# Kernel tuning notes

Measured on AMD Instinct MI355X. Metric: run time of the kernel, lower is better.

Reference implementation:

```python
import jax, jax.numpy as jnp
import numpy as np

B, L, D = 2, 2048, 2048
NH, HD = 16, 128
SCALE = HD ** -0.5


def setup_inputs() -> dict:
    key = jax.random.key(0)
    ks = jax.random.split(key, 9)
    s = D ** -0.5  # roughly torch Linear init scale
    return {
        "hidden_states": jax.random.normal(ks[0], (B, L, D), dtype=jnp.float32),
        "Wq": jax.random.normal(ks[1], (NH * HD, D), dtype=jnp.float32) * s,
        "bq": jnp.zeros((NH * HD,), dtype=jnp.float32),
        "Wk": jax.random.normal(ks[2], (NH * HD, D), dtype=jnp.float32) * s,
        "bk": jnp.zeros((NH * HD,), dtype=jnp.float32),
        "Wv": jax.random.normal(ks[3], (NH * HD, D), dtype=jnp.float32) * s,
        "bv": jnp.zeros((NH * HD,), dtype=jnp.float32),
        "Wo": jax.random.normal(ks[4], (D, NH * HD), dtype=jnp.float32) * s,
        "bo": jnp.zeros((D,), dtype=jnp.float32),
    }


def reference(hidden_states, Wq, bq, Wk, bk, Wv, bv, Wo, bo):
    # projections (torch Linear: x @ W.T + b), split into heads: b s h d
    q = (hidden_states @ Wq.T + bq).reshape(B, L, NH, HD)
    k = (hidden_states @ Wk.T + bk).reshape(B, L, NH, HD)
    v = (hidden_states @ Wv.T + bv).reshape(B, L, NH, HD)
    # scores: [B, NH, L, L]
    scores = jnp.einsum("bqhd,bkhd->bhqk", q, k) * SCALE
    causal = jnp.tril(jnp.ones((L, L), dtype=bool))  # True = keep
    scores = jnp.where(causal, scores, jnp.float32(-jnp.inf))
    probs = jax.nn.softmax(scores, axis=-1)
    out = jnp.einsum("bhqk,bkhd->bqhd", probs, v).reshape(B, L, NH * HD)
    return out @ Wo.T + bo
```

## Files before the change

### kernel.cpp

```cpp
#include <hip/hip_runtime.h>

#define B_  2
#define L_  2048
#define D_  2048
#define NH_ 16
#define HD_ 128

typedef __bf16 bf16_t;
typedef __bf16 bf16x8 __attribute__((ext_vector_type(8)));
typedef __bf16 bf16x4 __attribute__((ext_vector_type(4)));
typedef float  f32x4  __attribute__((ext_vector_type(4)));

typedef const __attribute__((address_space(1))) void* gas_ptr;
typedef __attribute__((address_space(3))) void* las_ptr;

__device__ __forceinline__ void g2l16(const void* g, void* l) {
    __builtin_amdgcn_global_load_lds((gas_ptr)g, (las_ptr)l, 16, 0, 0);
}

__device__ __forceinline__ void raw_barrier() {
    asm volatile("s_barrier" ::: "memory");
}
__device__ __forceinline__ void wait_vm8() {
    asm volatile("s_waitcnt vmcnt(8)" ::: "memory");
}
__device__ __forceinline__ void wait_vm4() {
    asm volatile("s_waitcnt vmcnt(4)" ::: "memory");
}
__device__ __forceinline__ void wait_vm2() {
    asm volatile("s_waitcnt vmcnt(2)" ::: "memory");
}
__device__ __forceinline__ void wait_vm0() {
    asm volatile("s_waitcnt vmcnt(0)" ::: "memory");
}

__global__ __launch_bounds__(256) void cvt_all(const float* __restrict__ X,
                                               const float* __restrict__ Wq,
                                               const float* __restrict__ Wk,
                                               const float* __restrict__ Wv,
                                               const float* __restrict__ Wo,
                                               bf16_t* __restrict__ Xb,
                                               bf16_t* __restrict__ Wqkvb,
                                               bf16_t* __restrict__ Wob) {
    int i = blockIdx.x * 256 + threadIdx.x;
    const float* src;
    bf16_t* dst;
    int off;
    if (i < 2097152) { src = X; dst = Xb; off = i; }
    else {
        int j = i - 2097152;
        int w = j >> 20;
        off = j & 1048575;
        src = (w == 0) ? Wq : (w == 1) ? Wk : (w == 2) ? Wv : Wo;
        dst = (w == 3) ? Wob : Wqkvb + (size_t)w * 4194304;
    }
    float4 v = ((const float4*)src)[off];
    bf16x4 o;
    o[0] = (bf16_t)v.x; o[1] = (bf16_t)v.y; o[2] = (bf16_t)v.z; o[3] = (bf16_t)v.w;
    ((bf16x4*)dst)[off] = o;
}

__global__ __launch_bounds__(256) void gemm_bt(const bf16_t* __restrict__ A,
                                               const bf16_t* __restrict__ Bw,
                                               const float* __restrict__ bias,
                                               float* __restrict__ C,
                                               int M, int N, int K) {
    constexpr int BK = 32;
    __shared__ __align__(16) bf16_t smem[16384];
    const int tid  = threadIdx.x;
    const int wave = tid >> 6, lane = tid & 63;
    const int quad = lane >> 4, l16 = lane & 15;
    const int tm = blockIdx.y * 128, tn = blockIdx.x * 128;
    const int wm = (wave >> 1) * 64, wn = (wave & 1) * 64;

    const int srow = wave * 16 + (lane >> 2);
    const int scol = (lane & 3) * 8;
    const bf16_t* Ag = A  + (size_t)(tm + srow) * K + scol;
    const bf16_t* Bg = Bw + (size_t)(tn + srow) * K + scol;
    const size_t rowskip = (size_t)64 * K;

    auto stage = [&](int k0, int p) {
        bf16_t* a = smem + p * 4096 + (wave * 16) * BK;
        bf16_t* bl = smem + 8192 + p * 4096 + (wave * 16) * BK;
        g2l16(Ag + k0, a);
        g2l16(Ag + k0 + rowskip, a + 64 * BK);
        g2l16(Bg + k0, bl);
        g2l16(Bg + k0 + rowskip, bl + 64 * BK);
    };

    f32x4 acc[4][4] = {};
    const int niter = K / BK;
    stage(0, 0);

    for (int i = 0; i < niter; ++i) {
        const int p = i & 1;
        if (i + 1 < niter) { stage((i + 1) * BK, p ^ 1); wait_vm4(); }
        else wait_vm0();
        raw_barrier();

        const bf16_t* Alp = smem + p * 4096;
        const bf16_t* Blp = smem + 8192 + p * 4096;
        bf16x8 af[4], bf[4];
#pragma unroll
        for (int ii = 0; ii < 4; ++ii)
            af[ii] = *(const bf16x8*)(Alp + (wm + ii * 16 + l16) * BK + quad * 8);
#pragma unroll
        for (int j = 0; j < 4; ++j)
            bf[j] = *(const bf16x8*)(Blp + (wn + j * 16 + l16) * BK + quad * 8);
#pragma unroll
        for (int ii = 0; ii < 4; ++ii)
#pragma unroll
            for (int j = 0; j < 4; ++j)
                acc[ii][j] = __builtin_amdgcn_mfma_f32_16x16x32_bf16(af[ii], bf[j], acc[ii][j], 0, 0, 0);
        raw_barrier();
    }

#pragma unroll
    for (int j = 0; j < 4; ++j) {
        const int col = tn + wn + j * 16 + l16;
        const float bv = bias[col];
#pragma unroll
        for (int i = 0; i < 4; ++i) {
            const int row0 = tm + wm + i * 16 + quad * 4;
#pragma unroll
            for (int r = 0; r < 4; ++r)
                C[(size_t)(row0 + r) * N + col] = acc[i][j][r] + bv;
        }
    }
}

__global__ __launch_bounds__(512, 2) void gemm_qk(const bf16_t* __restrict__ A,
                                                  const bf16_t* __restrict__ Bw,
                                                  const float* __restrict__ b0,
                                                  const float* __restrict__ b1,
                                                  bf16_t* __restrict__ QK) {
    constexpr int K  = D_;
    constexpr int BK = 64;
    constexpr int NT = K / BK;
    __shared__ __align__(16) bf16_t smem[65536];

    const int tid  = threadIdx.x;
    const int wave = tid >> 6, lane = tid & 63;
    const int quad = lane >> 4, l16 = lane & 15;
    const int tm = blockIdx.y * 256, tn = blockIdx.x * 256;
    const int wm = (wave >> 2) * 128;
    const int wn = (wave & 3) * 64;
    const int seg = tn >> 11;

    const int srow = tid >> 3;
    const int sg   = (tid & 7) ^ (srow & 7);
    const bf16_t* Ag = A  + (size_t)(tm + srow) * K + sg * 8;
    const bf16_t* Bg = Bw + (size_t)(tn + srow) * K + sg * 8;
    const int ldsw = wave * 512;

    auto stageA = [&](int t, int h) {
        bf16_t* l = smem + (t & 1) * 32768 + h * 8192 + ldsw;
        const bf16_t* g = Ag + (size_t)h * 128 * K + t * BK;
        g2l16(g, l);
        g2l16(g + (size_t)64 * K, l + 4096);
    };
    auto stageB = [&](int t, int h) {
        bf16_t* l = smem + (t & 1) * 32768 + 16384 + h * 8192 + ldsw;
        const bf16_t* g = Bg + (size_t)h * 128 * K + t * BK;
        g2l16(g, l);
        g2l16(g + (size_t)64 * K, l + 4096);
    };

    f32x4 acc[8][4] = {};

    stageA(0, 0); stageA(0, 1); stageB(0, 0); stageB(0, 1);

    const int abase_w = (wave >> 2) * 8192;
    const int bbase_w = 16384 + ((wave >> 1) & 1) * 8192;
    const int brow0   = (wave & 1) * 64;

    for (int t = 0; t < NT; ++t) {
        const int p = t & 1;
        const bf16_t* Ah = smem + p * 32768 + abase_w;
        const bf16_t* Bh = smem + p * 32768 + bbase_w;
        bf16x8 af[4][2], bfr[2][2], bfr2[2][2];

        raw_barrier();
        if (t + 1 < NT) { stageA(t + 1, 0); wait_vm2(); }
        else wait_vm0();
        raw_barrier();

#pragma unroll
        for (int mb = 0; mb < 4; ++mb)
#pragma unroll
            for (int ks = 0; ks < 2; ++ks) {
                const int row = mb * 16 + l16;
                af[mb][ks] = *(const bf16x8*)(Ah + row * 64 + (((ks * 4 + quad) ^ (row & 7)) << 3));
            }
#pragma unroll
        for (int nb = 0; nb < 2; ++nb)
#pragma unroll
            for (int ks = 0; ks < 2; ++ks) {
                const int row = brow0 + nb * 16 + l16;
                bfr[nb][ks] = *(const bf16x8*)(Bh + row * 64 + (((ks * 4 + quad) ^ (row & 7)) << 3));
            }
        __builtin_amdgcn_s_setprio(1);
#pragma unroll
        for (int mb = 0; mb < 4; ++mb)
#pragma unroll
            for (int nb = 0; nb < 2; ++nb)
#pragma unroll
                for (int ks = 0; ks < 2; ++ks)
                    acc[mb][nb] = __builtin_amdgcn_mfma_f32_16x16x32_bf16(af[mb][ks], bfr[nb][ks], acc[mb][nb], 0, 0, 0);
        __builtin_amdgcn_s_setprio(0);

        if (t + 1 < NT) stageA(t + 1, 1);
#pragma unroll
        for (int nb = 0; nb < 2; ++nb)
#pragma unroll
            for (int ks = 0; ks < 2; ++ks) {
                const int row = brow0 + (nb + 2) * 16 + l16;
                bfr2[nb][ks] = *(const bf16x8*)(Bh + row * 64 + (((ks * 4 + quad) ^ (row & 7)) << 3));
            }
        raw_barrier();
        __builtin_amdgcn_s_setprio(1);
#pragma unroll
        for (int mb = 0; mb < 4; ++mb)
#pragma unroll
            for (int nb = 0; nb < 2; ++nb)
#pragma unroll
                for (int ks = 0; ks < 2; ++ks)
                    acc[mb][nb + 2] = __builtin_amdgcn_mfma_f32_16x16x32_bf16(af[mb][ks], bfr2[nb][ks], acc[mb][nb + 2], 0, 0, 0);
        __builtin_amdgcn_s_setprio(0);

        if (t + 1 < NT) stageB(t + 1, 0);
#pragma unroll
        for (int mb = 0; mb < 4; ++mb)
#pragma unroll
            for (int ks = 0; ks < 2; ++ks) {
                const int row = (mb + 4) * 16 + l16;
                af[mb][ks] = *(const bf16x8*)(Ah + row * 64 + (((ks * 4 + quad) ^ (row & 7)) << 3));
            }
        raw_barrier();
        __builtin_amdgcn_s_setprio(1);
#pragma unroll
        for (int mb = 0; mb < 4; ++mb)
#pragma unroll
            for (int nb = 0; nb < 2; ++nb)
#pragma unroll
                for (int ks = 0; ks < 2; ++ks)
                    acc[mb + 4][nb + 2] = __builtin_amdgcn_mfma_f32_16x16x32_bf16(af[mb][ks], bfr2[nb][ks], acc[mb + 4][nb + 2], 0, 0, 0);
        __builtin_amdgcn_s_setprio(0);

        if (t + 1 < NT) stageB(t + 1, 1);
#pragma unroll
        for (int nb = 0; nb < 2; ++nb)
#pragma unroll
            for (int ks = 0; ks < 2; ++ks) {
                const int row = brow0 + nb * 16 + l16;
                bfr[nb][ks] = *(const bf16x8*)(Bh + row * 64 + (((ks * 4 + quad) ^ (row & 7)) << 3));
            }
        raw_barrier();
        __builtin_amdgcn_s_setprio(1);
#pragma unroll
        for (int mb = 0; mb < 4; ++mb)
#pragma unroll
            for (int nb = 0; nb < 2; ++nb)
#pragma unroll
                for (int ks = 0; ks < 2; ++ks)
                    acc[mb + 4][nb] = __builtin_amdgcn_mfma_f32_16x16x32_bf16(af[mb][ks], bfr[nb][ks], acc[mb + 4][nb], 0, 0, 0);
        __builtin_amdgcn_s_setprio(0);
    }

    const float* bias = (seg == 0) ? b0 : b1;
#pragma unroll
    for (int nb = 0; nb < 4; ++nb) {
        const int col = tn + wn + nb * 16 + l16;
        const float bv = bias[col & 2047];
#pragma unroll
        for (int mb = 0; mb < 8; ++mb) {
            const int row0 = tm + wm + mb * 16 + quad * 4;
#pragma unroll
            for (int r = 0; r < 4; ++r)
                QK[(size_t)(row0 + r) * 4096 + col] = (bf16_t)(acc[mb][nb][r] + bv);
        }
    }
}

__global__ __launch_bounds__(512, 2) void gemm_v(const bf16_t* __restrict__ A,
                                                 const bf16_t* __restrict__ Bv,
                                                 const float* __restrict__ b2,
                                                 bf16_t* __restrict__ Vt) {
    constexpr int K  = D_;
    constexpr int BK = 64;
    constexpr int NT = K / BK;
    __shared__ __align__(16) bf16_t smem[49152];

    const int tid  = threadIdx.x;
    const int wave = tid >> 6, lane = tid & 63;
    const int quad = lane >> 4, l16 = lane & 15;
    const int hx = blockIdx.x;
    const int tm = blockIdx.y * 256;
    const int wm = (wave >> 1) * 64;
    const int wn = (wave & 1) * 64;

    const int srow = tid >> 3;
    const int sg   = (tid & 7) ^ (srow & 7);
    const bf16_t* Ag = A  + (size_t)(tm + srow) * K + sg * 8;
    const bf16_t* Bg = Bv + (size_t)(hx * 128 + srow) * K + sg * 8;
    const int ldsw = wave * 512;

    auto stageVA = [&](int t, int q) {
        bf16_t* l = smem + (t & 1) * 24576 + q * 4096 + ldsw;
        g2l16(Ag + (size_t)q * 64 * K + t * BK, l);
    };
    auto stageVB = [&](int t, int q) {
        bf16_t* l = smem + (t & 1) * 24576 + 16384 + q * 4096 + ldsw;
        g2l16(Bg + (size_t)q * 64 * K + t * BK, l);
    };

    f32x4 acc[4][4] = {};

    stageVA(0, 0); stageVA(0, 1); stageVA(0, 2); stageVA(0, 3);
    stageVB(0, 0); stageVB(0, 1);

    for (int t = 0; t < NT; ++t) {
        const int p = t & 1;
        const bf16_t* Ah = smem + p * 24576;
        const bf16_t* Bl = smem + p * 24576 + 16384;
        bf16x8 af0[4], af1[4], bf0[2], bf1[2], bf2[2], bf3[2];

        raw_barrier();
        if (t + 1 < NT) { stageVA(t + 1, 0); stageVA(t + 1, 1); wait_vm2(); }
        else wait_vm0();
        raw_barrier();

#pragma unroll
        for (int mb = 0; mb < 4; ++mb) {
            const int row = wm + mb * 16 + l16;
            af0[mb] = *(const bf16x8*)(Ah + row * 64 + ((quad ^ (row & 7)) << 3));
        }
#pragma unroll
        for (int nb = 0; nb < 2; ++nb) {
            const int row = wn + nb * 16 + l16;
            bf0[nb] = *(const bf16x8*)(Bl + row * 64 + ((quad ^ (row & 7)) << 3));
        }
        __builtin_amdgcn_s_setprio(1);
#pragma unroll
        for (int mb = 0; mb < 4; ++mb)
#pragma unroll
            for (int nb = 0; nb < 2; ++nb)
                acc[mb][nb] = __builtin_amdgcn_mfma_f32_16x16x32_bf16(af0[mb], bf0[nb], acc[mb][nb], 0, 0, 0);
        __builtin_amdgcn_s_setprio(0);

        if (t + 1 < NT) { stageVA(t + 1, 2); stageVB(t + 1, 0); }
#pragma unroll
        for (int nb = 0; nb < 2; ++nb) {
            const int row = wn + (nb + 2) * 16 + l16;
            bf1[nb] = *(const bf16x8*)(Bl + row * 64 + ((quad ^ (row & 7)) << 3));
        }
        raw_barrier();
        __builtin_amdgcn_s_setprio(1);
#pragma unroll
        for (int mb = 0; mb < 4; ++mb)
#pragma unroll
            for (int nb = 0; nb < 2; ++nb)
                acc[mb][nb + 2] = __builtin_amdgcn_mfma_f32_16x16x32_bf16(af0[mb], bf1[nb], acc[mb][nb + 2], 0, 0, 0);
        __builtin_amdgcn_s_setprio(0);

        if (t + 1 < NT) { stageVA(t + 1, 3); stageVB(t + 1, 1); }
#pragma unroll
        for (int mb = 0; mb < 4; ++mb) {
            const int row = wm + mb * 16 + l16;
            af1[mb] = *(const bf16x8*)(Ah + row * 64 + (((4 + quad) ^ (row & 7)) << 3));
        }
#pragma unroll
        for (int nb = 0; nb < 2; ++nb) {
            const int row = wn + (nb + 2) * 16 + l16;
            bf2[nb] = *(const bf16x8*)(Bl + row * 64 + (((4 + quad) ^ (row & 7)) << 3));
        }
        raw_barrier();
        __builtin_amdgcn_s_setprio(1);
#pragma unroll
        for (int mb = 0; mb < 4; ++mb)
#pragma unroll
            for (int nb = 0; nb < 2; ++nb)
                acc[mb][nb + 2] = __builtin_amdgcn_mfma_f32_16x16x32_bf16(af1[mb], bf2[nb], acc[mb][nb + 2], 0, 0, 0);
        __builtin_amdgcn_s_setprio(0);

#pragma unroll
        for (int nb = 0; nb < 2; ++nb) {
            const int row = wn + nb * 16 + l16;
            bf3[nb] = *(const bf16x8*)(Bl + row * 64 + (((4 + quad) ^ (row & 7)) << 3));
        }
        raw_barrier();
        __builtin_amdgcn_s_setprio(1);
#pragma unroll
        for (int mb = 0; mb < 4; ++mb)
#pragma unroll
            for (int nb = 0; nb < 2; ++nb)
                acc[mb][nb] = __builtin_amdgcn_mfma_f32_16x16x32_bf16(af1[mb], bf3[nb], acc[mb][nb], 0, 0, 0);
        __builtin_amdgcn_s_setprio(0);
    }

    __syncthreads();
    bf16_t* Tw = smem + wave * 4096;
    const int b = tm >> 11;
    const int tokbase = tm & 2047;
#pragma unroll
    for (int nb = 0; nb < 4; ++nb) {
        const int dloc = nb * 16 + l16;
        const float bv = b2[hx * 128 + wn + dloc];
#pragma unroll
        for (int mb = 0; mb < 4; ++mb)
#pragma unroll
            for (int r = 0; r < 4; ++r) {
                const int tokl = mb * 16 + quad * 4 + r;
                Tw[dloc * 64 + ((((tokl >> 3) ^ (dloc & 7)) << 3) | (tokl & 7))] =
                    (bf16_t)(acc[mb][nb][r] + bv);
            }
    }
    const int dl = lane;
    bf16_t* gp = Vt + ((size_t)(b * NH_ + hx) * HD_ + wn + dl) * L_ + tokbase + wm;
#pragma unroll
    for (int c = 0; c < 8; ++c) {
        bf16x8 v = *(const bf16x8*)(Tw + dl * 64 + ((c ^ (dl & 7)) << 3));
        *(bf16x8*)(gp + c * 8) = v;
    }
}

__global__ __launch_bounds__(256, 2) void attn_kernel(const bf16_t* __restrict__ QK,
                                                      const bf16_t* __restrict__ Vt,
                                                      bf16_t* __restrict__ Ctx) {
    constexpr float SCALE = 0.08838834764831845f;
    constexpr float MFIX  = 8.0f;
    const int bid = blockIdx.x;
    const int bh = bid & 31;
    const int qt = 15 - (bid >> 5);
    const int b = bh >> 4, h = bh & 15;
    const int tid = threadIdx.x, wave = tid >> 6, lane = tid & 63;
    const int quad = lane >> 4, l16 = lane & 15;
    const int q0 = qt * 128;

    __shared__ bf16_t Kl[2][64 * 128];
    __shared__ bf16_t Vl[2][128 * 64];
    __shared__ bf16_t Pl[4][16 * 72];

    bf16x8 qf[2][4];
#pragma unroll
    for (int s = 0; s < 2; ++s) {
        const bf16_t* qp = QK + (size_t)(b * L_ + q0 + wave * 32 + s * 16 + l16) * 4096 + h * HD_ + quad * 8;
#pragma unroll
        for (int ks = 0; ks < 4; ++ks) qf[s][ks] = *(const bf16x8*)(qp + ks * 32);
    }

    bf16x8 ones;
#pragma unroll
    for (int j = 0; j < 8; ++j) ones[j] = (bf16_t)1.0f;

    f32x4 oacc[2][8] = {};
    f32x4 lacc[2] = {};

    const bf16_t* Kg = QK + (size_t)(b * L_) * 4096 + 2048 + h * HD_;
    const bf16_t* Vg = Vt + (size_t)(bh * HD_) * L_;

    auto stage = [&](int tile, int p) {
        const bf16_t* kg = Kg + (size_t)tile * 64 * 4096;
        const bf16_t* vg = Vg + tile * 64;
#pragma unroll
        for (int c = 0; c < 4; ++c) {
            int row = c * 16 + wave * 4 + (lane >> 4);
            int gcol = ((lane & 15) ^ (row & 15)) * 8;
            g2l16(kg + (size_t)row * 4096 + gcol, &Kl[p][(c * 16 + wave * 4) * 128]);
        }
#pragma unroll
        for (int c = 0; c < 4; ++c) {
            int row = c * 32 + wave * 8 + (lane >> 3);
            int gcol = ((lane & 7) ^ (row & 7)) * 8;
            g2l16(vg + (size_t)row * L_ + gcol, &Vl[p][(c * 32 + wave * 8) * 64]);
        }
    };

    const int n = 2 * qt + 2;
    stage(0, 0);

    for (int it = 0; it < n; ++it) {
        const int p = it & 1;
        if (it + 1 < n) {
            stage(it + 1, p ^ 1);
            wait_vm8();
        } else {
            wait_vm0();
        }
        raw_barrier();

        const int kb = it * 64;
        const bool need_mask = (it >= n - 2);

        f32x4 sa[2][4] = {};
#pragma unroll
        for (int nt = 0; nt < 4; ++nt) {
            const int krow = nt * 16 + l16;
#pragma unroll
            for (int ks = 0; ks < 4; ++ks) {
                bf16x8 kf = *(const bf16x8*)(&Kl[p][krow * 128 + (((ks * 4 + quad) ^ l16) * 8)]);
                sa[0][nt] = __builtin_amdgcn_mfma_f32_16x16x32_bf16(qf[0][ks], kf, sa[0][nt], 0, 0, 0);
                sa[1][nt] = __builtin_amdgcn_mfma_f32_16x16x32_bf16(qf[1][ks], kf, sa[1][nt], 0, 0, 0);
            }
        }

        bf16x8 pf0[2], pf1[2];
#pragma unroll
        for (int nt = 0; nt < 4; ++nt)
#pragma unroll
            for (int r = 0; r < 4; ++r) {
                float sv = sa[0][nt][r] * SCALE - MFIX;
                if (need_mask) {
                    const int key = kb + nt * 16 + l16;
                    const int qq = q0 + wave * 32 + quad * 4 + r;
                    sv = (key <= qq) ? sv : -1e30f;
                }
                Pl[wave][(quad * 4 + r) * 72 + nt * 16 + l16] = (bf16_t)__expf(sv);
            }
        pf0[0] = *(const bf16x8*)(&Pl[wave][l16 * 72 + quad * 8]);
        pf0[1] = *(const bf16x8*)(&Pl[wave][l16 * 72 + 32 + quad * 8]);

#pragma unroll
        for (int nt = 0; nt < 4; ++nt)
#pragma unroll
            for (int r = 0; r < 4; ++r) {
                float sv = sa[1][nt][r] * SCALE - MFIX;
                if (need_mask) {
                    const int key = kb + nt * 16 + l16;
                    const int qq = q0 + wave * 32 + 16 + quad * 4 + r;
                    sv = (key <= qq) ? sv : -1e30f;
                }
                Pl[wave][(quad * 4 + r) * 72 + nt * 16 + l16] = (bf16_t)__expf(sv);
            }
        pf1[0] = *(const bf16x8*)(&Pl[wave][l16 * 72 + quad * 8]);
        pf1[1] = *(const bf16x8*)(&Pl[wave][l16 * 72 + 32 + quad * 8]);

        lacc[0] = __builtin_amdgcn_mfma_f32_16x16x32_bf16(pf0[0], ones, lacc[0], 0, 0, 0);
        lacc[0] = __builtin_amdgcn_mfma_f32_16x16x32_bf16(pf0[1], ones, lacc[0], 0, 0, 0);
        lacc[1] = __builtin_amdgcn_mfma_f32_16x16x32_bf16(pf1[0], ones, lacc[1], 0, 0, 0);
        lacc[1] = __builtin_amdgcn_mfma_f32_16x16x32_bf16(pf1[1], ones, lacc[1], 0, 0, 0);

#pragma unroll
        for (int dt = 0; dt < 8; ++dt) {
            const int drow = dt * 16 + l16;
#pragma unroll
            for (int ks = 0; ks < 2; ++ks) {
                bf16x8 vf = *(const bf16x8*)(&Vl[p][drow * 64 + (((ks * 4 + quad) ^ (drow & 7)) * 8)]);
                oacc[0][dt] = __builtin_amdgcn_mfma_f32_16x16x32_bf16(pf0[ks], vf, oacc[0][dt], 0, 0, 0);
                oacc[1][dt] = __builtin_amdgcn_mfma_f32_16x16x32_bf16(pf1[ks], vf, oacc[1][dt], 0, 0, 0);
            }
        }
        raw_barrier();
    }

#pragma unroll
    for (int s = 0; s < 2; ++s)
#pragma unroll
        for (int r = 0; r < 4; ++r) {
            const float inv = 1.0f / lacc[s][r];
            const int q = q0 + wave * 32 + s * 16 + quad * 4 + r;
            bf16_t* cp = Ctx + (size_t)(b * L_ + q) * 2048 + h * HD_;
#pragma unroll
            for (int dt = 0; dt < 8; ++dt)
                cp[dt * 16 + l16] = (bf16_t)(oacc[s][dt][r] * inv);
        }
}

extern "C" void kernel_launch(void* const* d_in, const int* in_sizes, int n_in,
                              void* d_out, int out_size, void* d_ws, size_t ws_size,
                              hipStream_t stream) {
    const float* X  = (const float*)d_in[0];
    const float* Wq = (const float*)d_in[1];
    const float* bq = (const float*)d_in[2];
    const float* Wk = (const float*)d_in[3];
    const float* bk = (const float*)d_in[4];
    const float* Wv = (const float*)d_in[5];
    const float* bv = (const float*)d_in[6];
    const float* Wo = (const float*)d_in[7];
    const float* bo = (const float*)d_in[8];
    float* out = (float*)d_out;

    char* ws = (char*)d_ws;
    bf16_t* Xb   = (bf16_t*)(ws);
    bf16_t* Ctx  = (bf16_t*)(ws);
    bf16_t* Wqkv = (bf16_t*)(ws + 16777216);
    bf16_t* Wob  = (bf16_t*)(ws + 41943040);
    bf16_t* QKb  = (bf16_t*)(ws + 50331648);
    bf16_t* Vtb  = (bf16_t*)(ws + 83886080);

    cvt_all<<<24576, 256, 0, stream>>>(X, Wq, Wk, Wv, Wo, Xb, Wqkv, Wob);

    gemm_qk<<<dim3(16, 16), 512, 0, stream>>>(Xb, Wqkv, bq, bk, QKb);

    gemm_v<<<dim3(16, 16), 512, 0, stream>>>(Xb, Wqkv + 8388608, bv, Vtb);

    attn_kernel<<<dim3(512), 256, 0, stream>>>(QKb, Vtb, Ctx);

    gemm_bt<<<dim3(16, 32), 256, 0, stream>>>(Ctx, Wob, bo, out,
                                              B_ * L_, D_, D_);
}
```

Baseline: 359.8 us.

## Replace output GEMM with pipelined swizzled kernel and streamline attention softmax

```diff
diff --git a/kernel.cpp b/kernel.cpp
--- a/kernel.cpp
+++ b/kernel.cpp
@@ -24,14 +24,17 @@
 __device__ __forceinline__ void wait_vm8() {
     asm volatile("s_waitcnt vmcnt(8)" ::: "memory");
 }
-__device__ __forceinline__ void wait_vm4() {
-    asm volatile("s_waitcnt vmcnt(4)" ::: "memory");
-}
 __device__ __forceinline__ void wait_vm2() {
     asm volatile("s_waitcnt vmcnt(2)" ::: "memory");
 }
 __device__ __forceinline__ void wait_vm0() {
     asm volatile("s_waitcnt vmcnt(0)" ::: "memory");
+}
+
+__device__ __forceinline__ float hw_exp2(float x) {
+    float r;
+    asm("v_exp_f32 %0, %1" : "=v"(r) : "v"(x));
+    return r;
 }
 
 __global__ __launch_bounds__(256) void cvt_all(const float* __restrict__ X,
@@ -60,75 +63,6 @@
     ((bf16x4*)dst)[off] = o;
 }
 
-__global__ __launch_bounds__(256) void gemm_bt(const bf16_t* __restrict__ A,
-                                               const bf16_t* __restrict__ Bw,
-                                               const float* __restrict__ bias,
-                                               float* __restrict__ C,
-                                               int M, int N, int K) {
-    constexpr int BK = 32;
-    __shared__ __align__(16) bf16_t smem[16384];
-    const int tid  = threadIdx.x;
-    const int wave = tid >> 6, lane = tid & 63;
-    const int quad = lane >> 4, l16 = lane & 15;
-    const int tm = blockIdx.y * 128, tn = blockIdx.x * 128;
-    const int wm = (wave >> 1) * 64, wn = (wave & 1) * 64;
-
-    const int srow = wave * 16 + (lane >> 2);
-    const int scol = (lane & 3) * 8;
-    const bf16_t* Ag = A  + (size_t)(tm + srow) * K + scol;
-    const bf16_t* Bg = Bw + (size_t)(tn + srow) * K + scol;
-    const size_t rowskip = (size_t)64 * K;
-
-    auto stage = [&](int k0, int p) {
-        bf16_t* a = smem + p * 4096 + (wave * 16) * BK;
-        bf16_t* bl = smem + 8192 + p * 4096 + (wave * 16) * BK;
-        g2l16(Ag + k0, a);
-        g2l16(Ag + k0 + rowskip, a + 64 * BK);
-        g2l16(Bg + k0, bl);
-        g2l16(Bg + k0 + rowskip, bl + 64 * BK);
-    };
-
-    f32x4 acc[4][4] = {};
-    const int niter = K / BK;
-    stage(0, 0);
-
-    for (int i = 0; i < niter; ++i) {
-        const int p = i & 1;
-        if (i + 1 < niter) { stage((i + 1) * BK, p ^ 1); wait_vm4(); }
-        else wait_vm0();
-        raw_barrier();
-
-        const bf16_t* Alp = smem + p * 4096;
-        const bf16_t* Blp = smem + 8192 + p * 4096;
-        bf16x8 af[4], bf[4];
-#pragma unroll
-        for (int ii = 0; ii < 4; ++ii)
-            af[ii] = *(const bf16x8*)(Alp + (wm + ii * 16 + l16) * BK + quad * 8);
-#pragma unroll
-        for (int j = 0; j < 4; ++j)
-            bf[j] = *(const bf16x8*)(Blp + (wn + j * 16 + l16) * BK + quad * 8);
-#pragma unroll
-        for (int ii = 0; ii < 4; ++ii)
-#pragma unroll
-            for (int j = 0; j < 4; ++j)
-                acc[ii][j] = __builtin_amdgcn_mfma_f32_16x16x32_bf16(af[ii], bf[j], acc[ii][j], 0, 0, 0);
-        raw_barrier();
-    }
-
-#pragma unroll
-    for (int j = 0; j < 4; ++j) {
-        const int col = tn + wn + j * 16 + l16;
-        const float bv = bias[col];
-#pragma unroll
-        for (int i = 0; i < 4; ++i) {
-            const int row0 = tm + wm + i * 16 + quad * 4;
-#pragma unroll
-            for (int r = 0; r < 4; ++r)
-                C[(size_t)(row0 + r) * N + col] = acc[i][j][r] + bv;
-        }
-    }
-}
-
 __global__ __launch_bounds__(512, 2) void gemm_qk(const bf16_t* __restrict__ A,
                                                   const bf16_t* __restrict__ Bw,
                                                   const float* __restrict__ b0,
@@ -143,8 +77,6 @@
     const int wave = tid >> 6, lane = tid & 63;
     const int quad = lane >> 4, l16 = lane & 15;
     const int tm = blockIdx.y * 256, tn = blockIdx.x * 256;
-    const int wm = (wave >> 2) * 128;
-    const int wn = (wave & 3) * 64;
     const int seg = tn >> 11;
 
     const int srow = tid >> 3;
@@ -267,6 +199,8 @@
         __builtin_amdgcn_s_setprio(0);
     }
 
+    const int wm = (wave >> 2) * 128;
+    const int wn = (wave & 3) * 64;
     const float* bias = (seg == 0) ? b0 : b1;
 #pragma unroll
     for (int nb = 0; nb < 4; ++nb) {
@@ -424,11 +358,141 @@
     }
 }
 
+__global__ __launch_bounds__(512, 2) void gemm_o(const bf16_t* __restrict__ A,
+                                                 const bf16_t* __restrict__ Bw,
+                                                 const float* __restrict__ bias,
+                                                 float* __restrict__ C) {
+    constexpr int K  = D_;
+    constexpr int BK = 64;
+    constexpr int NT = K / BK;
+    __shared__ __align__(16) bf16_t smem[49152];
+
+    const int tid  = threadIdx.x;
+    const int wave = tid >> 6, lane = tid & 63;
+    const int quad = lane >> 4, l16 = lane & 15;
+    const int tn = blockIdx.x * 128;
+    const int tm = blockIdx.y * 256;
+    const int wm = (wave >> 1) * 64;
+    const int wn = (wave & 1) * 64;
+
+    const int srow = tid >> 3;
+    const int sg   = (tid & 7) ^ (srow & 7);
+    const bf16_t* Ag = A  + (size_t)(tm + srow) * K + sg * 8;
+    const bf16_t* Bg = Bw + (size_t)(tn + srow) * K + sg * 8;
+    const int ldsw = wave * 512;
+
+    auto stageVA = [&](int t, int q) {
+        bf16_t* l = smem + (t & 1) * 24576 + q * 4096 + ldsw;
+        g2l16(Ag + (size_t)q * 64 * K + t * BK, l);
+    };
+    auto stageVB = [&](int t, int q) {
+        bf16_t* l = smem + (t & 1) * 24576 + 16384 + q * 4096 + ldsw;
+        g2l16(Bg + (size_t)q * 64 * K + t * BK, l);
+    };
+
+    f32x4 acc[4][4] = {};
+
+    stageVA(0, 0); stageVA(0, 1); stageVA(0, 2); stageVA(0, 3);
+    stageVB(0, 0); stageVB(0, 1);
+
+    for (int t = 0; t < NT; ++t) {
+        const int p = t & 1;
+        const bf16_t* Ah = smem + p * 24576;
+        const bf16_t* Bl = smem + p * 24576 + 16384;
+        bf16x8 af0[4], af1[4], bf0[2], bf1[2], bf2[2], bf3[2];
+
+        raw_barrier();
+        if (t + 1 < NT) { stageVA(t + 1, 0); stageVA(t + 1, 1); wait_vm2(); }
+        else wait_vm0();
+        raw_barrier();
+
+#pragma unroll
+        for (int mb = 0; mb < 4; ++mb) {
+            const int row = wm + mb * 16 + l16;
+            af0[mb] = *(const bf16x8*)(Ah + row * 64 + ((quad ^ (row & 7)) << 3));
+        }
+#pragma unroll
+        for (int nb = 0; nb < 2; ++nb) {
+            const int row = wn + nb * 16 + l16;
+            bf0[nb] = *(const bf16x8*)(Bl + row * 64 + ((quad ^ (row & 7)) << 3));
+        }
+        __builtin_amdgcn_s_setprio(1);
+#pragma unroll
+        for (int mb = 0; mb < 4; ++mb)
+#pragma unroll
+            for (int nb = 0; nb < 2; ++nb)
+                acc[mb][nb] = __builtin_amdgcn_mfma_f32_16x16x32_bf16(af0[mb], bf0[nb], acc[mb][nb], 0, 0, 0);
+        __builtin_amdgcn_s_setprio(0);
+
+        if (t + 1 < NT) { stageVA(t + 1, 2); stageVB(t + 1, 0); }
+#pragma unroll
+        for (int nb = 0; nb < 2; ++nb) {
+            const int row = wn + (nb + 2) * 16 + l16;
+            bf1[nb] = *(const bf16x8*)(Bl + row * 64 + ((quad ^ (row & 7)) << 3));
+        }
+        raw_barrier();
+        __builtin_amdgcn_s_setprio(1);
+#pragma unroll
+        for (int mb = 0; mb < 4; ++mb)
+#pragma unroll
+            for (int nb = 0; nb < 2; ++nb)
+                acc[mb][nb + 2] = __builtin_amdgcn_mfma_f32_16x16x32_bf16(af0[mb], bf1[nb], acc[mb][nb + 2], 0, 0, 0);
+        __builtin_amdgcn_s_setprio(0);
+
+        if (t + 1 < NT) { stageVA(t + 1, 3); stageVB(t + 1, 1); }
+#pragma unroll
+        for (int mb = 0; mb < 4; ++mb) {
+            const int row = wm + mb * 16 + l16;
+            af1[mb] = *(const bf16x8*)(Ah + row * 64 + (((4 + quad) ^ (row & 7)) << 3));
+        }
+#pragma unroll
+        for (int nb = 0; nb < 2; ++nb) {
+            const int row = wn + (nb + 2) * 16 + l16;
+            bf2[nb] = *(const bf16x8*)(Bl + row * 64 + (((4 + quad) ^ (row & 7)) << 3));
+        }
+        raw_barrier();
+        __builtin_amdgcn_s_setprio(1);
+#pragma unroll
+        for (int mb = 0; mb < 4; ++mb)
+#pragma unroll
+            for (int nb = 0; nb < 2; ++nb)
+                acc[mb][nb + 2] = __builtin_amdgcn_mfma_f32_16x16x32_bf16(af1[mb], bf2[nb], acc[mb][nb + 2], 0, 0, 0);
+        __builtin_amdgcn_s_setprio(0);
+
+#pragma unroll
+        for (int nb = 0; nb < 2; ++nb) {
+            const int row = wn + nb * 16 + l16;
+            bf3[nb] = *(const bf16x8*)(Bl + row * 64 + (((4 + quad) ^ (row & 7)) << 3));
+        }
+        raw_barrier();
+        __builtin_amdgcn_s_setprio(1);
+#pragma unroll
+        for (int mb = 0; mb < 4; ++mb)
+#pragma unroll
+            for (int nb = 0; nb < 2; ++nb)
+                acc[mb][nb] = __builtin_amdgcn_mfma_f32_16x16x32_bf16(af1[mb], bf3[nb], acc[mb][nb], 0, 0, 0);
+        __builtin_amdgcn_s_setprio(0);
+    }
+
+#pragma unroll
+    for (int nb = 0; nb < 4; ++nb) {
+        const int col = tn + wn + nb * 16 + l16;
+        const float bv = bias[col];
+#pragma unroll
+        for (int mb = 0; mb < 4; ++mb) {
+            const int row0 = tm + wm + mb * 16 + quad * 4;
+#pragma unroll
+            for (int r = 0; r < 4; ++r)
+                C[(size_t)(row0 + r) * 2048 + col] = acc[mb][nb][r] + bv;
+        }
+    }
+}
+
 __global__ __launch_bounds__(256, 2) void attn_kernel(const bf16_t* __restrict__ QK,
                                                       const bf16_t* __restrict__ Vt,
                                                       bf16_t* __restrict__ Ctx) {
-    constexpr float SCALE = 0.08838834764831845f;
-    constexpr float MFIX  = 8.0f;
+    constexpr float C1 = 0.12751838257308022f;
+    constexpr float C2n = -11.541560327111707f;
     const int bid = blockIdx.x;
     const int bh = bid & 31;
     const int qt = 15 - (bid >> 5);
@@ -477,6 +541,7 @@
     };
 
     const int n = 2 * qt + 2;
+    const int qb = q0 + wave * 32;
     stage(0, 0);
 
     for (int it = 0; it < n; ++it) {
@@ -491,65 +556,90 @@
 
         const int kb = it * 64;
         const bool need_mask = (it >= n - 2);
+        const bool a00 = (kb      <= qb + 15);
+        const bool a01 = (kb + 32 <= qb + 15);
+        const bool a10 = (kb      <= qb + 31);
+        const bool a11 = (kb + 32 <= qb + 31);
 
         f32x4 sa[2][4] = {};
+        __builtin_amdgcn_s_setprio(1);
 #pragma unroll
         for (int nt = 0; nt < 4; ++nt) {
+            const bool aO = (nt < 2) ? a10 : a11;
+            const bool aI = (nt < 2) ? a00 : a01;
+            if (!aO) continue;
             const int krow = nt * 16 + l16;
 #pragma unroll
             for (int ks = 0; ks < 4; ++ks) {
                 bf16x8 kf = *(const bf16x8*)(&Kl[p][krow * 128 + (((ks * 4 + quad) ^ l16) * 8)]);
-                sa[0][nt] = __builtin_amdgcn_mfma_f32_16x16x32_bf16(qf[0][ks], kf, sa[0][nt], 0, 0, 0);
-                sa[1][nt] = __builtin_amdgcn_mfma_f32_16x16x32_bf16(qf[1][ks], kf, sa[1][nt], 0, 0, 0);
-            }
-        }
+                if (aI) sa[0][nt] = __builtin_amdgcn_mfma_f32_16x16x32_bf16(kf, qf[0][ks], sa[0][nt], 0, 0, 0);
+                sa[1][nt] = __builtin_amdgcn_mfma_f32_16x16x32_bf16(kf, qf[1][ks], sa[1][nt], 0, 0, 0);
+            }
+        }
+        __builtin_amdgcn_s_setprio(0);
 
         bf16x8 pf0[2], pf1[2];
-#pragma unroll
-        for (int nt = 0; nt < 4; ++nt)
-#pragma unroll
-            for (int r = 0; r < 4; ++r) {
-                float sv = sa[0][nt][r] * SCALE - MFIX;
+        const int qq0 = qb + l16;
+        const int qq1 = qb + 16 + l16;
+#pragma unroll
+        for (int nt = 0; nt < 4; ++nt) {
+            if (!((nt < 2) ? a00 : a01)) continue;
+#pragma unroll
+            for (int rp = 0; rp < 2; ++rp) {
+                float e0 = hw_exp2(fmaf(sa[0][nt][2 * rp],     C1, C2n));
+                float e1 = hw_exp2(fmaf(sa[0][nt][2 * rp + 1], C1, C2n));
                 if (need_mask) {
-                    const int key = kb + nt * 16 + l16;
-                    const int qq = q0 + wave * 32 + quad * 4 + r;
-                    sv = (key <= qq) ? sv : -1e30f;
+                    const int k0 = kb + nt * 16 + quad * 4 + 2 * rp;
+                    e0 = (k0     <= qq0) ? e0 : 0.0f;
+                    e1 = (k0 + 1 <= qq0) ? e1 : 0.0f;
                 }
-                Pl[wave][(quad * 4 + r) * 72 + nt * 16 + l16] = (bf16_t)__expf(sv);
-            }
-        pf0[0] = *(const bf16x8*)(&Pl[wave][l16 * 72 + quad * 8]);
-        pf0[1] = *(const bf16x8*)(&Pl[wave][l16 * 72 + 32 + quad * 8]);
-
-#pragma unroll
-        for (int nt = 0; nt < 4; ++nt)
-#pragma unroll
-            for (int r = 0; r < 4; ++r) {
-                float sv = sa[1][nt][r] * SCALE - MFIX;
+                unsigned int pk;
+                asm("v_cvt_pk_bf16_f32 %0, %1, %2" : "=v"(pk) : "v"(e0), "v"(e1));
+                *(unsigned int*)(&Pl[wave][l16 * 72 + nt * 16 + quad * 4 + 2 * rp]) = pk;
+            }
+        }
+        if (a00) pf0[0] = *(const bf16x8*)(&Pl[wave][l16 * 72 + quad * 8]);
+        if (a01) pf0[1] = *(const bf16x8*)(&Pl[wave][l16 * 72 + 32 + quad * 8]);
+
+#pragma unroll
+        for (int nt = 0; nt < 4; ++nt) {
+            if (!((nt < 2) ? a10 : a11)) continue;
+#pragma unroll
+            for (int rp = 0; rp < 2; ++rp) {
+                float e0 = hw_exp2(fmaf(sa[1][nt][2 * rp],     C1, C2n));
+                float e1 = hw_exp2(fmaf(sa[1][nt][2 * rp + 1], C1, C2n));
                 if (need_mask) {
-                    const int key = kb + nt * 16 + l16;
-                    const int qq = q0 + wave * 32 + 16 + quad * 4 + r;
-                    sv = (key <= qq) ? sv : -1e30f;
+                    const int k0 = kb + nt * 16 + quad * 4 + 2 * rp;
+                    e0 = (k0     <= qq1) ? e0 : 0.0f;
+                    e1 = (k0 + 1 <= qq1) ? e1 : 0.0f;
                 }
-                Pl[wave][(quad * 4 + r) * 72 + nt * 16 + l16] = (bf16_t)__expf(sv);
-            }
-        pf1[0] = *(const bf16x8*)(&Pl[wave][l16 * 72 + quad * 8]);
-        pf1[1] = *(const bf16x8*)(&Pl[wave][l16 * 72 + 32 + quad * 8]);
-
-        lacc[0] = __builtin_amdgcn_mfma_f32_16x16x32_bf16(pf0[0], ones, lacc[0], 0, 0, 0);
-        lacc[0] = __builtin_amdgcn_mfma_f32_16x16x32_bf16(pf0[1], ones, lacc[0], 0, 0, 0);
-        lacc[1] = __builtin_amdgcn_mfma_f32_16x16x32_bf16(pf1[0], ones, lacc[1], 0, 0, 0);
-        lacc[1] = __builtin_amdgcn_mfma_f32_16x16x32_bf16(pf1[1], ones, lacc[1], 0, 0, 0);
-
+                unsigned int pk;
+                asm("v_cvt_pk_bf16_f32 %0, %1, %2" : "=v"(pk) : "v"(e0), "v"(e1));
+                *(unsigned int*)(&Pl[wave][l16 * 72 + nt * 16 + quad * 4 + 2 * rp]) = pk;
+            }
+        }
+        if (a10) pf1[0] = *(const bf16x8*)(&Pl[wave][l16 * 72 + quad * 8]);
+        if (a11) pf1[1] = *(const bf16x8*)(&Pl[wave][l16 * 72 + 32 + quad * 8]);
+
+        if (a00) lacc[0] = __builtin_amdgcn_mfma_f32_16x16x32_bf16(pf0[0], ones, lacc[0], 0, 0, 0);
+        if (a01) lacc[0] = __builtin_amdgcn_mfma_f32_16x16x32_bf16(pf0[1], ones, lacc[0], 0, 0, 0);
+        if (a10) lacc[1] = __builtin_amdgcn_mfma_f32_16x16x32_bf16(pf1[0], ones, lacc[1], 0, 0, 0);
+        if (a11) lacc[1] = __builtin_amdgcn_mfma_f32_16x16x32_bf16(pf1[1], ones, lacc[1], 0, 0, 0);
+
+        __builtin_amdgcn_s_setprio(1);
 #pragma unroll
         for (int dt = 0; dt < 8; ++dt) {
             const int drow = dt * 16 + l16;
 #pragma unroll
             for (int ks = 0; ks < 2; ++ks) {
+                if (!(ks ? a11 : a10)) continue;
                 bf16x8 vf = *(const bf16x8*)(&Vl[p][drow * 64 + (((ks * 4 + quad) ^ (drow & 7)) * 8)]);
-                oacc[0][dt] = __builtin_amdgcn_mfma_f32_16x16x32_bf16(pf0[ks], vf, oacc[0][dt], 0, 0, 0);
+                if (ks ? a01 : a00)
+                    oacc[0][dt] = __builtin_amdgcn_mfma_f32_16x16x32_bf16(pf0[ks], vf, oacc[0][dt], 0, 0, 0);
                 oacc[1][dt] = __builtin_amdgcn_mfma_f32_16x16x32_bf16(pf1[ks], vf, oacc[1][dt], 0, 0, 0);
             }
         }
+        __builtin_amdgcn_s_setprio(0);
         raw_barrier();
     }
 
@@ -596,6 +686,5 @@
 
     attn_kernel<<<dim3(512), 256, 0, stream>>>(QKb, Vtb, Ctx);
 
-    gemm_bt<<<dim3(16, 32), 256, 0, stream>>>(Ctx, Wob, bo, out,
-                                              B_ * L_, D_, D_);
-}
+    gemm_o<<<dim3(16, 16), 512, 0, stream>>>(Ctx, Wob, bo, out);
+}
```

Measured after the change: 390.9 us. 1.09x slower.
